# Kernel tuning notes

Hardware: AMD Instinct MI355X
Metric: run time of the kernel (lower is better)

Reference implementation:

```python
import jax, jax.numpy as jnp
import numpy as np

MODES = 16

def _spectral_conv(x, w1r, w1i, w2r, w2i):
    # x: [N, Cin, R, R]; weights: [Cin, Cout, MODES, MODES] (real/imag parts)
    N, Cin, R, _ = x.shape
    Cout = w1r.shape[1]
    x_ft = jnp.fft.rfft2(x, axes=(-2, -1))  # [N, Cin, R, R//2+1] complex
    w1 = w1r + 1j * w1i
    w2 = w2r + 1j * w2i
    top = jnp.einsum('ncxy,coxy->noxy', x_ft[:, :, :MODES, :MODES], w1)
    bot = jnp.einsum('ncxy,coxy->noxy', x_ft[:, :, -MODES:, :MODES], w2)
    out_ft = jnp.zeros((N, Cout, R, R // 2 + 1), dtype=x_ft.dtype)
    out_ft = out_ft.at[:, :, :MODES, :MODES].set(top)
    out_ft = out_ft.at[:, :, -MODES:, :MODES].set(bot)
    return jnp.fft.irfft2(out_ft, s=(R, R), axes=(-2, -1))

def _forward(ref, w1r, w1i, w2r, w2i, subdomain_lookup):
    B, S, C, R, _ = ref.shape
    x = ref.reshape(B * S, C, R, R)
    # spectral conv + residual for ALL subdomains at once (vectorizes the torch loop)
    u_sub = _spectral_conv(x, w1r, w1i, w2r, w2i) + x  # [B*S, C, R, R]
    flat = u_sub.reshape(B, S, C, R * R)
    idx = subdomain_lookup.reshape(-1)  # [R*R], values in [0, S)
    pos = jnp.arange(R * R)
    # per-pixel select of owning subdomain: u[b, c, p] = flat[b, idx[p], c, p]
    # advanced indices (idx, pos) separated by a slice move to the front -> [R*R, B, C]
    u = flat[:, idx, :, pos]
    return jnp.transpose(u, (1, 2, 0)).reshape(B, C, R, R)

def setup_inputs():
    key = jax.random.key(0)
    ks = jax.random.split(key, 7)
    B, S, C, R, M = 4, 16, 64, 128, MODES
    scale = 1.0 / (C * C)
    return {
        'reference': jax.random.normal(ks[0], (B, S, C, R, R), dtype=jnp.float32),
        'physical_coords': jax.random.normal(ks[1], (2, R, R), dtype=jnp.float32),
        'subdomain_lookup': jax.random.randint(ks[2], (R, R), 0, S),
        'w1r': scale * jax.random.normal(ks[3], (C, C, M, M), dtype=jnp.float32),
        'w1i': scale * jax.random.normal(ks[4], (C, C, M, M), dtype=jnp.float32),
        'w2r': scale * jax.random.normal(ks[5], (C, C, M, M), dtype=jnp.float32),
        'w2i': scale * jax.random.normal(ks[6], (C, C, M, M), dtype=jnp.float32),
    }

def reference(reference, physical_coords, subdomain_lookup, w1r, w1i, w2r, w2i):
    del physical_coords  # only used for shape checks / dead ref_grid in the original
    return _forward(reference, w1r, w1i, w2r, w2i, subdomain_lookup)
```

## Files before the change

### kernel.cpp

```cpp
#include <hip/hip_runtime.h>
#include <math.h>


#define TWO_PI_OVER_128 0.04908738521234052f
#define RCAP 1280

typedef __attribute__((ext_vector_type(8))) short bf16x8;
typedef __attribute__((ext_vector_type(4))) float f32x4;
union FragU { uint4 u; bf16x8 s; };

__device__ __forceinline__ unsigned pk(float a, float b) {
  unsigned ua = __float_as_uint(a), ub = __float_as_uint(b);
  ua = (ua + 0x7FFFu + ((ua >> 16) & 1u)) >> 16;
  ub = (ub + 0x7FFFu + ((ub >> 16) & 1u)) >> 16;
  return ua | (ub << 16);
}
__device__ __forceinline__ float2 upk(unsigned v) {
  return make_float2(__uint_as_float(v << 16), __uint_as_float(v & 0xFFFF0000u));
}
__device__ __forceinline__ unsigned bf1(float a) {
  unsigned ua = __float_as_uint(a);
  return (ua + 0x7FFFu + ((ua >> 16) & 1u)) >> 16;
}

__global__ __launch_bounds__(1024) void kprep(const int* __restrict__ lu,
                                              int* __restrict__ scomb,
                                              int* __restrict__ plist,
                                              int* __restrict__ cntg,
                                              int* __restrict__ cnthg,
                                              unsigned* __restrict__ Etu,
                                              unsigned* __restrict__ Gtu,
                                              unsigned* __restrict__ G2tu,
                                              const float* __restrict__ w1r,
                                              const float* __restrict__ w1i,
                                              const float* __restrict__ w2r,
                                              const float* __restrict__ w2i,
                                              unsigned* __restrict__ Wt) {
  __shared__ int wsum[16];
  __shared__ unsigned tile[64 * 65];
  const int blk = blockIdx.x;
  const int tid = threadIdx.x;
  if (blk < 16) {
    const int s = blk;
    const int lane = tid & 63, wid = tid >> 6;
    const int4* lu4 = (const int4*)lu + tid * 4;
    unsigned match = 0;
#pragma unroll
    for (int q = 0; q < 4; ++q) {
      int4 v = lu4[q];
      match |= (v.x == s ? 1u : 0u) << (4 * q);
      match |= (v.y == s ? 1u : 0u) << (4 * q + 1);
      match |= (v.z == s ? 1u : 0u) << (4 * q + 2);
      match |= (v.w == s ? 1u : 0u) << (4 * q + 3);
    }
    const int cnt = __popc(match);
    int pre = cnt;
#pragma unroll
    for (int d = 1; d < 64; d <<= 1) {
      int t = __shfl_up(pre, d, 64);
      if (lane >= d) pre += t;
    }
    if (lane == 63) wsum[wid] = pre;
    __syncthreads();
    int woff = 0;
    for (int j = 0; j < wid; ++j) woff += wsum[j];
    int r = woff + pre - cnt;
    if (tid == 512) cnthg[s] = r;
    const int base = tid * 16;
#pragma unroll
    for (int i = 0; i < 16; ++i) {
      if ((match >> i) & 1u) {
        const int p = base + i;
        scomb[p] = (s << 12) | r;
        if (r < RCAP) plist[s * RCAP + r] = p;
        ++r;
      }
    }
    if (tid == 1023) {
      const int tot = woff + pre;
      cntg[s] = (tot < RCAP) ? tot : RCAP;
    }
  } else if (blk == 16) {
    for (int i = 0; i < 2; ++i) {
      int t = i * 1024 + tid;
      int w = t >> 6, y0 = (t & 63) * 2;
      float v[2];
#pragma unroll
      for (int q = 0; q < 2; ++q) {
        int y = y0 + q;
        if (w < 16) v[q] = cosf((float)((w * y) & 127) * TWO_PI_OVER_128);
        else        v[q] = -sinf((float)(((w - 16) * y) & 127) * TWO_PI_OVER_128);
      }
      Etu[t] = bf1(v[0]) | (bf1(v[1]) << 16);
    }
    for (int i = 0; i < 4; ++i) {
      int t = i * 1024 + tid;
      int jr = t >> 6, x0 = (t & 63) * 2;
      int j = (jr & 31);
      int kx = (j < 16) ? j : 96 + j;
      float v[2];
#pragma unroll
      for (int q = 0; q < 2; ++q) {
        int x = x0 + q;
        float a = (float)((kx * x) & 127) * TWO_PI_OVER_128;
        v[q] = (jr < 32) ? cosf(a) : sinf(a);
      }
      Gtu[t] = bf1(v[0]) | (bf1(v[1]) << 16);
    }
    for (int i = 0; i < 4; ++i) {
      int t = i * 1024 + tid;
      int x = t >> 5, k2 = t & 31;
      float v[2];
#pragma unroll
      for (int q = 0; q < 2; ++q) {
        int k = k2 * 2 + q;
        int kxi = k & 31;
        int kxe = (kxi < 16) ? kxi : 96 + kxi;
        float a = (float)((kxe * x) & 127) * TWO_PI_OVER_128;
        v[q] = (k < 32) ? cosf(a) : sinf(a);
      }
      G2tu[t] = bf1(v[0]) | (bf1(v[1]) << 16);
    }
  } else {
    const int ob = blk - 17;
    const int o = ob & 63, wsel = ob >> 6;
    const float* Wr = wsel ? w2r : w1r;
    const float* Wi = wsel ? w2i : w1i;
    for (int mc = 0; mc < 4; ++mc) {
      if (mc) __syncthreads();
      for (int i = 0; i < 4; ++i) {
        int idx = i * 1024 + tid;
        int c = idx >> 6, ml = idx & 63;
        int mh = mc * 64 + ml;
        float wsc = ((mh & 15) ? 2.f : 1.f) / 16384.f;
        size_t off = (size_t)(c * 64 + o) * 256 + mh;
        tile[c * 65 + ml] = pk(Wr[off] * wsc, Wi[off] * wsc);
      }
      __syncthreads();
      for (int i = 0; i < 4; ++i) {
        int idx = i * 1024 + tid;
        int ml = idx >> 6, c = idx & 63;
        Wt[(size_t)(wsel * 256 + mc * 64 + ml) * 4096 + o * 64 + c] = tile[c * 65 + ml];
      }
    }
  }
}

__global__ __launch_bounds__(256, 4) void k1_fwd(const float* __restrict__ ref,
                                                 const unsigned* __restrict__ Etu,
                                                 const unsigned* __restrict__ Gtu,
                                                 const int* __restrict__ cntg,
                                                 const int* __restrict__ cnthg,
                                                 const int* __restrict__ plist,
                                                 unsigned short* __restrict__ Rcomp,
                                                 unsigned* __restrict__ Xf) {
  __shared__ unsigned short imgL[64 * 128];
  __shared__ unsigned short A1t[2][32 * 128];
  unsigned* Xout = (unsigned*)imgL;
  const int bid2 = blockIdx.x;
  const int n = bid2 >> 5, cp = bid2 & 31;
  const int c0 = cp * 2;
  const int b = n >> 4, s = n & 15;
  const int tid = threadIdx.x;
  const int l = tid & 63, w = tid >> 6;

  FragU Ef[2][4];
#pragma unroll
  for (int nt = 0; nt < 2; ++nt)
#pragma unroll
    for (int ks = 0; ks < 4; ++ks)
      Ef[nt][ks].u = *(const uint4*)&Etu[(nt * 16 + (l & 15)) * 64 + ks * 16 + (l >> 4) * 4];

  const int ns = cntg[s], nh = cnthg[s];
  const int* pl = plist + s * RCAP;
  const float* imf0 = ref + (size_t)((n << 6) + c0) * 16384;

  float4 v[8];
  {
    const float4* p = (const float4*)imf0;
#pragma unroll
    for (int i = 0; i < 8; ++i) v[i] = p[i * 256 + tid];
  }

  for (int st = 0; st < 4; ++st) {
    const int img = st >> 1, half = st & 1;
    if (st) __syncthreads();
#pragma unroll
    for (int i = 0; i < 8; ++i) {
      const int pl2 = (i * 256 + tid) * 4;
      const int xl = pl2 >> 7, y0 = pl2 & 127;
      const int chunk = (y0 >> 3) ^ (xl & 15);
      *(uint2*)&imgL[xl * 128 + chunk * 8 + (y0 & 7)] =
          make_uint2(pk(v[i].x, v[i].y), pk(v[i].z, v[i].w));
    }
    __syncthreads();
    if (st < 3) {
      const int st2 = st + 1;
      const float4* p = (const float4*)(imf0 + (st2 >> 1) * 16384 + (st2 & 1) * 8192);
#pragma unroll
      for (int i = 0; i < 8; ++i) v[i] = p[i * 256 + tid];
    }
    f32x4 acc1[2] = {};
    const int xl = w * 16 + (l & 15);
#pragma unroll
    for (int ks = 0; ks < 4; ++ks) {
      const int chunk = (ks * 4 + (l >> 4)) ^ (xl & 15);
      FragU a;
      a.u = *(const uint4*)&imgL[xl * 128 + chunk * 8];
#pragma unroll
      for (int nt = 0; nt < 2; ++nt)
        acc1[nt] = __builtin_amdgcn_mfma_f32_16x16x32_bf16(a.s, Ef[nt][ks].s, acc1[nt], 0, 0, 0);
    }
    {
      const int x0 = (half * 4 + w) * 16 + (l >> 4) * 4;
#pragma unroll
      for (int nt = 0; nt < 2; ++nt) {
        const int wp = nt * 16 + (l & 15);
        const int chunk = (x0 >> 3) ^ (wp & 15);
        *(uint2*)&A1t[img][wp * 128 + chunk * 8 + (x0 & 7)] =
            make_uint2(pk(acc1[nt][0], acc1[nt][1]), pk(acc1[nt][2], acc1[nt][3]));
      }
    }
    {
      unsigned short* rc = Rcomp + ((size_t)((b << 6) + c0 + img) * 16 + s) * RCAP;
      const int rlo = half ? nh : 0, rhi = half ? ns : nh;
      for (int r = rlo + tid; r < rhi; r += 256) {
        const int p = pl[r];
        const int gxl = (p >> 7) - half * 64, y = p & 127;
        rc[r] = imgL[gxl * 128 + (((y >> 3) ^ (gxl & 15))) * 8 + (y & 7)];
      }
    }
  }
  __syncthreads();

  {
    const int wi = w >> 1, wl = w & 1;
    FragU Gf[2];
    f32x4 acc2[2][2] = {};
#pragma unroll
    for (int ks = 0; ks < 4; ++ks) {
#pragma unroll
      for (int mtl = 0; mtl < 2; ++mtl)
        Gf[mtl].u = *(const uint4*)&Gtu[((wl + 2 * mtl) * 16 + (l & 15)) * 64 + ks * 16 + (l >> 4) * 4];
#pragma unroll
      for (int nt = 0; nt < 2; ++nt) {
        const int wp = nt * 16 + (l & 15);
        const int chunk = (ks * 4 + (l >> 4)) ^ (wp & 15);
        FragU bfr;
        bfr.u = *(const uint4*)&A1t[wi][wp * 128 + chunk * 8];
#pragma unroll
        for (int mtl = 0; mtl < 2; ++mtl)
          acc2[mtl][nt] = __builtin_amdgcn_mfma_f32_16x16x32_bf16(Gf[mtl].s, bfr.s, acc2[mtl][nt], 0, 0, 0);
      }
    }
#pragma unroll
    for (int r = 0; r < 4; ++r) {
      const int j = wl * 16 + (l >> 4) * 4 + r;
      const int ky = l & 15;
      const float re = acc2[0][0][r] + acc2[1][1][r];
      const float im = acc2[0][1][r] - acc2[1][0][r];
      Xout[wi * 512 + j * 16 + ky] = pk(re, im);
    }
  }
  __syncthreads();
  {
    uint2* dst = (uint2*)(Xf + (size_t)((n << 6) + c0) * 512);
    const uint2* src = (const uint2*)Xout;
    dst[tid] = src[tid];
    dst[tid + 256] = src[tid + 256];
  }
}

__global__ __launch_bounds__(256) void kt(const unsigned* __restrict__ Xf,
                                          unsigned* __restrict__ Xf2) {
  __shared__ unsigned tile[64 * 65];
  const int bm = blockIdx.x & 7, bn = blockIdx.x >> 3;
  const int tid = threadIdx.x;
  for (int i = 0; i < 16; ++i) {
    int idx = i * 256 + tid;
    int r = idx >> 6, cc = idx & 63;
    tile[r * 65 + cc] = Xf[(size_t)(bn * 64 + r) * 512 + bm * 64 + cc];
  }
  __syncthreads();
  for (int i = 0; i < 16; ++i) {
    int idx = i * 256 + tid;
    int r = idx >> 6, cc = idx & 63;
    Xf2[(size_t)(bm * 64 + r) * 4096 + bn * 64 + cc] = tile[cc * 65 + r];
  }
}

__global__ __launch_bounds__(256) void k2_mix(const unsigned* __restrict__ Xf2,
                                              const unsigned* __restrict__ Wt,
                                              unsigned* __restrict__ Yf) {
  __shared__ unsigned short Xr[64 * 64];
  __shared__ unsigned short Xi[64 * 64];
  __shared__ unsigned short Wr[64 * 64];
  __shared__ unsigned short Wi[64 * 64];
  const int m = blockIdx.x;
  const int tid = threadIdx.x;
  const int l = tid & 63, w = tid >> 6;
  for (int i = 0; i < 8; ++i) {
    const int e0 = (i * 256 + tid) * 2;
    const int n = e0 >> 6, cc = e0 & 63;
    const int pos = n * 64 + (((cc >> 3) ^ (n & 7)) << 3) + (cc & 7);
    uint2 xv = *(const uint2*)&Xf2[(size_t)m * 4096 + e0];
    *(unsigned*)&Xr[pos] = (xv.x & 0xFFFFu) | (xv.y << 16);
    *(unsigned*)&Xi[pos] = (xv.x >> 16) | (xv.y & 0xFFFF0000u);
    uint2 wv = *(const uint2*)&Wt[(size_t)m * 4096 + e0];
    *(unsigned*)&Wr[pos] = (wv.x & 0xFFFFu) | (wv.y << 16);
    *(unsigned*)&Wi[pos] = (wv.x >> 16) | (wv.y & 0xFFFF0000u);
  }
  __syncthreads();
  f32x4 acc[4][4] = {};
  const int arow = w * 16 + (l & 15);
#pragma unroll
  for (int ks = 0; ks < 2; ++ks) {
    FragU Ar, Ai;
    {
      const int chunk = ((ks * 4 + (l >> 4))) ^ (arow & 7);
      Ar.u = *(const uint4*)&Xr[arow * 64 + chunk * 8];
      Ai.u = *(const uint4*)&Xi[arow * 64 + chunk * 8];
    }
#pragma unroll
    for (int nt = 0; nt < 4; ++nt) {
      const int orow = nt * 16 + (l & 15);
      const int chunk = ((ks * 4 + (l >> 4))) ^ (orow & 7);
      FragU Br, Bi;
      Br.u = *(const uint4*)&Wr[orow * 64 + chunk * 8];
      Bi.u = *(const uint4*)&Wi[orow * 64 + chunk * 8];
      acc[nt][0] = __builtin_amdgcn_mfma_f32_16x16x32_bf16(Ar.s, Br.s, acc[nt][0], 0, 0, 0);
      acc[nt][1] = __builtin_amdgcn_mfma_f32_16x16x32_bf16(Ai.s, Bi.s, acc[nt][1], 0, 0, 0);
      acc[nt][2] = __builtin_amdgcn_mfma_f32_16x16x32_bf16(Ar.s, Bi.s, acc[nt][2], 0, 0, 0);
      acc[nt][3] = __builtin_amdgcn_mfma_f32_16x16x32_bf16(Ai.s, Br.s, acc[nt][3], 0, 0, 0);
    }
  }
#pragma unroll
  for (int nt = 0; nt < 4; ++nt) {
    unsigned o4[4];
#pragma unroll
    for (int r = 0; r < 4; ++r)
      o4[r] = pk(acc[nt][0][r] - acc[nt][1][r], acc[nt][2][r] + acc[nt][3][r]);
    const int bo = w * 64 + nt * 16 + (l & 15);
    *(uint4*)&Yf[(size_t)bo * 8192 + m * 16 + (l >> 4) * 4] = *(uint4*)o4;
  }
}

__global__ __launch_bounds__(1024, 4) void k3_inv(const unsigned* __restrict__ Yf,
                                                  const unsigned* __restrict__ G2tu,
                                                  const int* __restrict__ scomb,
                                                  const unsigned short* __restrict__ Rcomp,
                                                  float* __restrict__ out) {
  __shared__ __align__(16) unsigned short Ypb[16 * 32 * 40];
  __shared__ __align__(16) unsigned short tbuf[16 * 546];
  __shared__ float2 tab[128];
  const int bo = blockIdx.x >> 1, half = blockIdx.x & 1;
  const int tid = threadIdx.x;
  const int l = tid & 63, w = tid >> 6;
  if (tid < 128) {
    float sv, cv;
    sincosf((float)tid * TWO_PI_OVER_128, &sv, &cv);
    tab[tid] = make_float2(cv, sv);
  }
  {
    const unsigned* src = Yf + (size_t)bo * 8192;
    for (int i = 0; i < 8; ++i) {
      int e = i * 1024 + tid;
      unsigned v = src[e];
      int ss = e & 15, m = e >> 4, kxi = m >> 4, ky = m & 15;
      unsigned short* yb = Ypb + ss * 1280;
      yb[ky * 40 + kxi] = (unsigned short)(v & 0xFFFFu);
      yb[(16 + ky) * 40 + kxi] = (unsigned short)(v >> 16);
    }
  }
  __syncthreads();
  float* outb = out + (size_t)bo * 16384;
  const unsigned short* rcb = Rcomp + (size_t)bo * 16 * RCAP;
  unsigned* tb32 = (unsigned*)tbuf;

  for (int ch = 0; ch < 4; ++ch) {
    const int xb = half * 64 + ch * 16;
    {
      const int xg = xb + (l & 15);
      FragU Ac, As, B0, B1;
      Ac.u = *(const uint4*)&G2tu[xg * 32 + (l >> 4) * 4];
      As.u = *(const uint4*)&G2tu[xg * 32 + 16 + (l >> 4) * 4];
      const unsigned short* yb = Ypb + w * 1280;
      B0.u = *(const uint4*)&yb[(l & 15) * 40 + (l >> 4) * 8];
      B1.u = *(const uint4*)&yb[(16 + (l & 15)) * 40 + (l >> 4) * 8];
      f32x4 z = {};
      f32x4 d1  = __builtin_amdgcn_mfma_f32_16x16x32_bf16(Ac.s, B0.s, z, 0, 0, 0);
      f32x4 d1b = __builtin_amdgcn_mfma_f32_16x16x32_bf16(Ac.s, B1.s, z, 0, 0, 0);
      f32x4 d2  = __builtin_amdgcn_mfma_f32_16x16x32_bf16(As.s, B0.s, z, 0, 0, 0);
      f32x4 d2b = __builtin_amdgcn_mfma_f32_16x16x32_bf16(As.s, B1.s, z, 0, 0, 0);
      const int ky = l & 15;
#pragma unroll
      for (int r = 0; r < 4; ++r) {
        const int xloc = (l >> 4) * 4 + r;
        tb32[w * 273 + xloc * 17 + ky] = pk(d1[r] - d2b[r], d1b[r] + d2[r]);
      }
    }
    __syncthreads();
    {
      const int xg = xb + w;
      const int p0 = xg * 128 + l;
      const int sc0 = scomb[p0], sc1 = scomb[p0 + 64];
      const int ssa = sc0 >> 12, ssb = sc1 >> 12;
      const float r0 = __uint_as_float((unsigned)rcb[ssa * RCAP + (sc0 & 4095)] << 16);
      const float r1 = __uint_as_float((unsigned)rcb[ssb * RCAP + (sc1 & 4095)] << 16);
      const unsigned* tb0 = tb32 + ssa * 273 + w * 17;
      const unsigned* tb1 = tb32 + ssb * 273 + w * 17;
      const float2 stpy = tab[l];
      float acc0 = 0.f, acc1e = 0.f, acc1o = 0.f;
      float c0 = 1.f, s0 = 0.f;
#pragma unroll
      for (int k2 = 0; k2 < 16; ++k2) {
        const float2 ta = upk(tb0[k2]);
        const float2 tc = upk(tb1[k2]);
        acc0 = fmaf(ta.x, c0, fmaf(-ta.y, s0, acc0));
        if (k2 & 1) acc1o = fmaf(tc.x, c0, fmaf(-tc.y, s0, acc1o));
        else        acc1e = fmaf(tc.x, c0, fmaf(-tc.y, s0, acc1e));
        float nc = c0 * stpy.x - s0 * stpy.y, ns = s0 * stpy.x + c0 * stpy.y;
        c0 = nc; s0 = ns;
      }
      outb[p0] = r0 + acc0;
      outb[p0 + 64] = r1 + (acc1e - acc1o);
    }
    __syncthreads();
  }
}

extern "C" void kernel_launch(void* const* d_in, const int* in_sizes, int n_in,
                              void* d_out, int out_size, void* d_ws, size_t ws_size,
                              hipStream_t stream) {
  const float* ref = (const float*)d_in[0];
  const int* lu = (const int*)d_in[2];
  const float* w1r = (const float*)d_in[3];
  const float* w1i = (const float*)d_in[4];
  const float* w2r = (const float*)d_in[5];
  const float* w2i = (const float*)d_in[6];
  float* out = (float*)d_out;

  unsigned* Xf  = (unsigned*)d_ws;
  unsigned* Xf2 = Xf  + (size_t)4096 * 512;
  unsigned* Wt  = Xf2 + (size_t)4096 * 512;
  unsigned* Etu = Wt  + (size_t)4096 * 512;
  unsigned* Gtu = Etu + 2048;
  unsigned* G2tu = Gtu + 4096;
  int* cntg     = (int*)(G2tu + 4096);
  int* cnthg    = cntg + 16;
  int* plist    = cnthg + 16;
  int* scomb    = plist + 16 * RCAP;
  unsigned short* Rcomp = (unsigned short*)(scomb + 16384);
  unsigned* Yf  = Xf;

  kprep<<<145, 1024, 0, stream>>>(lu, scomb, plist, cntg, cnthg,
                                  Etu, Gtu, G2tu, w1r, w1i, w2r, w2i, Wt);
  k1_fwd<<<2048, 256, 0, stream>>>(ref, Etu, Gtu, cntg, cnthg, plist, Rcomp, Xf);
  kt<<<512, 256, 0, stream>>>(Xf, Xf2);
  k2_mix<<<512, 256, 0, stream>>>(Xf2, Wt, Yf);
  k3_inv<<<512, 1024, 0, stream>>>(Yf, G2tu, scomb, Rcomp, out);
}
```

Baseline: 113.1 us.

## Fold transpose into forward kernel and move weight prep into k1 blocks

Removes the separate transpose kernel by having k1_fwd write its spectral coefficients directly in a mode-grouped interleaved layout that k2_mix reads with strided loads. The weight repacking moves from the prep kernel into 128 extra blocks of k1_fwd, so that work overlaps with the forward transform and kprep shrinks to 17 blocks. It also drops the register prefetch of the next image slice in k1_fwd and loads inline instead. The trade-offs are scattered 4-byte global writes from k1, strided gathers in k2, and less load latency hiding in k1.

```diff
diff --git a/kernel.cpp b/kernel.cpp
--- a/kernel.cpp
+++ b/kernel.cpp
@@ -30,14 +30,8 @@
                                               int* __restrict__ cnthg,
                                               unsigned* __restrict__ Etu,
                                               unsigned* __restrict__ Gtu,
-                                              unsigned* __restrict__ G2tu,
-                                              const float* __restrict__ w1r,
-                                              const float* __restrict__ w1i,
-                                              const float* __restrict__ w2r,
-                                              const float* __restrict__ w2i,
-                                              unsigned* __restrict__ Wt) {
+                                              unsigned* __restrict__ G2tu) {
   __shared__ int wsum[16];
-  __shared__ unsigned tile[64 * 65];
   const int blk = blockIdx.x;
   const int tid = threadIdx.x;
   if (blk < 16) {
@@ -80,7 +74,7 @@
       const int tot = woff + pre;
       cntg[s] = (tot < RCAP) ? tot : RCAP;
     }
-  } else if (blk == 16) {
+  } else {
     for (int i = 0; i < 2; ++i) {
       int t = i * 1024 + tid;
       int w = t >> 6, y0 = (t & 63) * 2;
@@ -121,28 +115,6 @@
       }
       G2tu[t] = bf1(v[0]) | (bf1(v[1]) << 16);
     }
-  } else {
-    const int ob = blk - 17;
-    const int o = ob & 63, wsel = ob >> 6;
-    const float* Wr = wsel ? w2r : w1r;
-    const float* Wi = wsel ? w2i : w1i;
-    for (int mc = 0; mc < 4; ++mc) {
-      if (mc) __syncthreads();
-      for (int i = 0; i < 4; ++i) {
-        int idx = i * 1024 + tid;
-        int c = idx >> 6, ml = idx & 63;
-        int mh = mc * 64 + ml;
-        float wsc = ((mh & 15) ? 2.f : 1.f) / 16384.f;
-        size_t off = (size_t)(c * 64 + o) * 256 + mh;
-        tile[c * 65 + ml] = pk(Wr[off] * wsc, Wi[off] * wsc);
-      }
-      __syncthreads();
-      for (int i = 0; i < 4; ++i) {
-        int idx = i * 1024 + tid;
-        int ml = idx >> 6, c = idx & 63;
-        Wt[(size_t)(wsel * 256 + mc * 64 + ml) * 4096 + o * 64 + c] = tile[c * 65 + ml];
-      }
-    }
   }
 }
 
@@ -152,16 +124,49 @@
                                                  const int* __restrict__ cntg,
                                                  const int* __restrict__ cnthg,
                                                  const int* __restrict__ plist,
+                                                 const float* __restrict__ w1r,
+                                                 const float* __restrict__ w1i,
+                                                 const float* __restrict__ w2r,
+                                                 const float* __restrict__ w2i,
+                                                 unsigned* __restrict__ Wt,
                                                  unsigned short* __restrict__ Rcomp,
-                                                 unsigned* __restrict__ Xf) {
+                                                 unsigned* __restrict__ Xf2g) {
   __shared__ unsigned short imgL[64 * 128];
   __shared__ unsigned short A1t[2][32 * 128];
+  const int tid = threadIdx.x;
+
+  if (blockIdx.x >= 2048) {
+    unsigned* tileW = (unsigned*)imgL;
+    const int ob = blockIdx.x - 2048;
+    const int o = ob & 63, wsel = ob >> 6;
+    const float* Wr = wsel ? w2r : w1r;
+    const float* Wi = wsel ? w2i : w1i;
+    for (int mc = 0; mc < 4; ++mc) {
+      if (mc) __syncthreads();
+      for (int i = 0; i < 16; ++i) {
+        int idx = i * 256 + tid;
+        int c = idx >> 6, ml = idx & 63;
+        int mh = mc * 64 + ml;
+        float wsc = ((mh & 15) ? 2.f : 1.f) / 16384.f;
+        size_t off = (size_t)(c * 64 + o) * 256 + mh;
+        tileW[c * 64 + ((ml + c) & 63)] = pk(Wr[off] * wsc, Wi[off] * wsc);
+      }
+      __syncthreads();
+      for (int i = 0; i < 16; ++i) {
+        int idx = i * 256 + tid;
+        int ml = idx >> 6, c = idx & 63;
+        Wt[(size_t)(wsel * 256 + mc * 64 + ml) * 4096 + o * 64 + c] =
+            tileW[c * 64 + ((ml + c) & 63)];
+      }
+    }
+    return;
+  }
+
   unsigned* Xout = (unsigned*)imgL;
   const int bid2 = blockIdx.x;
   const int n = bid2 >> 5, cp = bid2 & 31;
   const int c0 = cp * 2;
   const int b = n >> 4, s = n & 15;
-  const int tid = threadIdx.x;
   const int l = tid & 63, w = tid >> 6;
 
   FragU Ef[2][4];
@@ -175,31 +180,20 @@
   const int* pl = plist + s * RCAP;
   const float* imf0 = ref + (size_t)((n << 6) + c0) * 16384;
 
-  float4 v[8];
-  {
-    const float4* p = (const float4*)imf0;
-#pragma unroll
-    for (int i = 0; i < 8; ++i) v[i] = p[i * 256 + tid];
-  }
-
   for (int st = 0; st < 4; ++st) {
     const int img = st >> 1, half = st & 1;
     if (st) __syncthreads();
+    const float4* im4 = (const float4*)(imf0 + img * 16384 + half * 8192);
 #pragma unroll
     for (int i = 0; i < 8; ++i) {
+      float4 v = im4[i * 256 + tid];
       const int pl2 = (i * 256 + tid) * 4;
       const int xl = pl2 >> 7, y0 = pl2 & 127;
       const int chunk = (y0 >> 3) ^ (xl & 15);
       *(uint2*)&imgL[xl * 128 + chunk * 8 + (y0 & 7)] =
-          make_uint2(pk(v[i].x, v[i].y), pk(v[i].z, v[i].w));
+          make_uint2(pk(v.x, v.y), pk(v.z, v.w));
     }
     __syncthreads();
-    if (st < 3) {
-      const int st2 = st + 1;
-      const float4* p = (const float4*)(imf0 + (st2 >> 1) * 16384 + (st2 & 1) * 8192);
-#pragma unroll
-      for (int i = 0; i < 8; ++i) v[i] = p[i * 256 + tid];
-    }
     f32x4 acc1[2] = {};
     const int xl = w * 16 + (l & 15);
 #pragma unroll
@@ -264,48 +258,41 @@
   }
   __syncthreads();
   {
-    uint2* dst = (uint2*)(Xf + (size_t)((n << 6) + c0) * 512);
-    const uint2* src = (const uint2*)Xout;
-    dst[tid] = src[tid];
-    dst[tid + 256] = src[tid + 256];
-  }
-}
-
-__global__ __launch_bounds__(256) void kt(const unsigned* __restrict__ Xf,
-                                          unsigned* __restrict__ Xf2) {
-  __shared__ unsigned tile[64 * 65];
-  const int bm = blockIdx.x & 7, bn = blockIdx.x >> 3;
-  const int tid = threadIdx.x;
-  for (int i = 0; i < 16; ++i) {
-    int idx = i * 256 + tid;
-    int r = idx >> 6, cc = idx & 63;
-    tile[r * 65 + cc] = Xf[(size_t)(bn * 64 + r) * 512 + bm * 64 + cc];
-  }
-  __syncthreads();
-  for (int i = 0; i < 16; ++i) {
-    int idx = i * 256 + tid;
-    int r = idx >> 6, cc = idx & 63;
-    Xf2[(size_t)(bm * 64 + r) * 4096 + bn * 64 + cc] = tile[cc * 65 + r];
-  }
-}
-
-__global__ __launch_bounds__(256) void k2_mix(const unsigned* __restrict__ Xf2,
+    const int bid0 = (n << 6) + c0;
+#pragma unroll
+    for (int k = 0; k < 4; ++k) {
+      const int idx = k * 256 + tid;
+      const int mg = idx >> 4, sub = idx & 15;
+      const int img = sub >> 3, ml = sub & 7;
+      Xf2g[((size_t)mg * 4096 + bid0 + img) * 8 + ml] = Xout[img * 512 + mg * 8 + ml];
+    }
+  }
+}
+
+__global__ __launch_bounds__(256) void k2_mix(const unsigned* __restrict__ Xf2g,
                                               const unsigned* __restrict__ Wt,
                                               unsigned* __restrict__ Yf) {
   __shared__ unsigned short Xr[64 * 64];
   __shared__ unsigned short Xi[64 * 64];
   __shared__ unsigned short Wr[64 * 64];
   __shared__ unsigned short Wi[64 * 64];
-  const int m = blockIdx.x;
+  const int mg = blockIdx.x & 63, ml = blockIdx.x >> 6;
+  const int m = mg * 8 + ml;
   const int tid = threadIdx.x;
   const int l = tid & 63, w = tid >> 6;
+  const unsigned* xsrc = Xf2g + (size_t)mg * 4096 * 8 + ml;
+  for (int i = 0; i < 16; ++i) {
+    const int e = i * 256 + tid;
+    const unsigned v = xsrc[(size_t)e * 8];
+    const int n = e >> 6, cc = e & 63;
+    const int pos = n * 64 + (((cc >> 3) ^ (n & 7)) << 3) + (cc & 7);
+    Xr[pos] = (unsigned short)(v & 0xFFFFu);
+    Xi[pos] = (unsigned short)(v >> 16);
+  }
   for (int i = 0; i < 8; ++i) {
     const int e0 = (i * 256 + tid) * 2;
     const int n = e0 >> 6, cc = e0 & 63;
     const int pos = n * 64 + (((cc >> 3) ^ (n & 7)) << 3) + (cc & 7);
-    uint2 xv = *(const uint2*)&Xf2[(size_t)m * 4096 + e0];
-    *(unsigned*)&Xr[pos] = (xv.x & 0xFFFFu) | (xv.y << 16);
-    *(unsigned*)&Xi[pos] = (xv.x >> 16) | (xv.y & 0xFFFF0000u);
     uint2 wv = *(const uint2*)&Wt[(size_t)m * 4096 + e0];
     *(unsigned*)&Wr[pos] = (wv.x & 0xFFFFu) | (wv.y << 16);
     *(unsigned*)&Wi[pos] = (wv.x >> 16) | (wv.y & 0xFFFF0000u);
@@ -440,23 +427,21 @@
   const float* w2i = (const float*)d_in[6];
   float* out = (float*)d_out;
 
-  unsigned* Xf  = (unsigned*)d_ws;
-  unsigned* Xf2 = Xf  + (size_t)4096 * 512;
-  unsigned* Wt  = Xf2 + (size_t)4096 * 512;
-  unsigned* Etu = Wt  + (size_t)4096 * 512;
-  unsigned* Gtu = Etu + 2048;
+  unsigned* Xf2g = (unsigned*)d_ws;
+  unsigned* Yf   = Xf2g + (size_t)64 * 4096 * 8;
+  unsigned* Wt   = Yf + (size_t)256 * 8192;
+  unsigned* Etu  = Wt + (size_t)512 * 4096;
+  unsigned* Gtu  = Etu + 2048;
   unsigned* G2tu = Gtu + 4096;
-  int* cntg     = (int*)(G2tu + 4096);
-  int* cnthg    = cntg + 16;
-  int* plist    = cnthg + 16;
-  int* scomb    = plist + 16 * RCAP;
+  int* cntg      = (int*)(G2tu + 4096);
+  int* cnthg     = cntg + 16;
+  int* plist     = cnthg + 16;
+  int* scomb     = plist + 16 * RCAP;
   unsigned short* Rcomp = (unsigned short*)(scomb + 16384);
-  unsigned* Yf  = Xf;
-
-  kprep<<<145, 1024, 0, stream>>>(lu, scomb, plist, cntg, cnthg,
-                                  Etu, Gtu, G2tu, w1r, w1i, w2r, w2i, Wt);
-  k1_fwd<<<2048, 256, 0, stream>>>(ref, Etu, Gtu, cntg, cnthg, plist, Rcomp, Xf);
-  kt<<<512, 256, 0, stream>>>(Xf, Xf2);
-  k2_mix<<<512, 256, 0, stream>>>(Xf2, Wt, Yf);
+
+  kprep<<<17, 1024, 0, stream>>>(lu, scomb, plist, cntg, cnthg, Etu, Gtu, G2tu);
+  k1_fwd<<<2176, 256, 0, stream>>>(ref, Etu, Gtu, cntg, cnthg, plist,
+                                   w1r, w1i, w2r, w2i, Wt, Rcomp, Xf2g);
+  k2_mix<<<512, 256, 0, stream>>>(Xf2g, Wt, Yf);
   k3_inv<<<512, 1024, 0, stream>>>(Yf, G2tu, scomb, Rcomp, out);
 }
```

New measurement: 138.2 us. +22.2%, slower.

## Use HIP bf16 conversion intrinsics and drop register prefetch of next image slab

Applied to the files above, without the earlier changes.

Replaces the hand-written round-to-nearest-even bf16 packing with the HIP library conversion intrinsics, which may map to hardware pack-convert instructions on this GPU. It also removes the software prefetch that loaded the next stage's float4 slab into registers during the MFMA work. Each stage now loads directly before writing to shared memory. This cuts register pressure, but global load latency is no longer hidden behind compute. NaN handling may differ from the manual rounding.

```diff
diff --git a/kernel.cpp b/kernel.cpp
--- a/kernel.cpp
+++ b/kernel.cpp
@@ -1,4 +1,5 @@
 #include <hip/hip_runtime.h>
+#include <hip/hip_bf16.h>
 #include <math.h>
 
 
@@ -10,17 +11,18 @@
 union FragU { uint4 u; bf16x8 s; };
 
 __device__ __forceinline__ unsigned pk(float a, float b) {
-  unsigned ua = __float_as_uint(a), ub = __float_as_uint(b);
-  ua = (ua + 0x7FFFu + ((ua >> 16) & 1u)) >> 16;
-  ub = (ub + 0x7FFFu + ((ub >> 16) & 1u)) >> 16;
-  return ua | (ub << 16);
+  __hip_bfloat162 h = __float22bfloat162_rn(make_float2(a, b));
+  union { __hip_bfloat162 h2; unsigned u; } cv;
+  cv.h2 = h;
+  return cv.u;
 }
 __device__ __forceinline__ float2 upk(unsigned v) {
   return make_float2(__uint_as_float(v << 16), __uint_as_float(v & 0xFFFF0000u));
 }
 __device__ __forceinline__ unsigned bf1(float a) {
-  unsigned ua = __float_as_uint(a);
-  return (ua + 0x7FFFu + ((ua >> 16) & 1u)) >> 16;
+  union { __hip_bfloat16 h; unsigned short u; } cv;
+  cv.h = __float2bfloat16(a);
+  return (unsigned)cv.u;
 }
 
 __global__ __launch_bounds__(1024) void kprep(const int* __restrict__ lu,
@@ -175,31 +177,20 @@
   const int* pl = plist + s * RCAP;
   const float* imf0 = ref + (size_t)((n << 6) + c0) * 16384;
 
-  float4 v[8];
-  {
-    const float4* p = (const float4*)imf0;
-#pragma unroll
-    for (int i = 0; i < 8; ++i) v[i] = p[i * 256 + tid];
-  }
-
   for (int st = 0; st < 4; ++st) {
     const int img = st >> 1, half = st & 1;
     if (st) __syncthreads();
+    const float4* im4 = (const float4*)(imf0 + img * 16384 + half * 8192);
 #pragma unroll
     for (int i = 0; i < 8; ++i) {
+      float4 v = im4[i * 256 + tid];
       const int pl2 = (i * 256 + tid) * 4;
       const int xl = pl2 >> 7, y0 = pl2 & 127;
       const int chunk = (y0 >> 3) ^ (xl & 15);
       *(uint2*)&imgL[xl * 128 + chunk * 8 + (y0 & 7)] =
-          make_uint2(pk(v[i].x, v[i].y), pk(v[i].z, v[i].w));
+          make_uint2(pk(v.x, v.y), pk(v.z, v.w));
     }
     __syncthreads();
-    if (st < 3) {
-      const int st2 = st + 1;
-      const float4* p = (const float4*)(imf0 + (st2 >> 1) * 16384 + (st2 & 1) * 8192);
-#pragma unroll
-      for (int i = 0; i < 8; ++i) v[i] = p[i * 256 + tid];
-    }
     f32x4 acc1[2] = {};
     const int xl = w * 16 + (l & 15);
 #pragma unroll
```

New measurement: 114.0 us. Within noise of the previous version (+0.7%).
